# Performance work log

Measured on AMD Instinct MI355X. Metric: run time of the kernel, lower is better.

## Reference

```python
import jax, jax.numpy as jnp
import numpy as np

B, J, E = 4096, 32, 256

def setup_inputs() -> dict:
    key = jax.random.key(0)
    ks = jax.random.split(key, 7)
    return {
        "x": jax.random.normal(ks[0], (B, E), dtype=jnp.float32),
        "state": jax.random.normal(ks[1], (B, J * E), dtype=jnp.float32),
        "keys": jax.random.normal(ks[2], (J, E), dtype=jnp.float32) * 0.1,
        "U": jax.random.normal(ks[3], (E, E), dtype=jnp.float32) * 0.1,
        "V": jax.random.normal(ks[4], (E, E), dtype=jnp.float32) * 0.1,
        "W": jax.random.normal(ks[5], (E, E), dtype=jnp.float32) * 0.1,
        "bias": jax.random.normal(ks[6], (E,), dtype=jnp.float32) * 0.1,
    }

def reference(x, state, keys, U, V, W, bias):
    b, je = state.shape
    j = keys.shape[0]
    e = x.shape[1]
    s = state.reshape(b, j, e)                      # [B,J,E]
    # gate_j = sigmoid(<x, state_j> + <x, key_j>)
    gate = jax.nn.sigmoid(jnp.einsum('be,bje->bj', x, s)
                          + x @ keys.T)             # [B,J]
    # candidate_j = relu(U s_j + bias + W x + V k_j)
    cand = jax.nn.relu(jnp.einsum('bje,fe->bjf', s, U)
                       + bias
                       + (x @ W.T)[:, None, :]
                       + (keys @ V.T)[None, :, :])  # [B,J,E]
    s_next = s + gate[..., None] * cand
    norm = jnp.abs(jnp.linalg.norm(s_next, axis=-1, keepdims=True)) + 1e-8
    s_next = s_next / norm
    return s_next.reshape(b, je)
```

## Files before the change

kernel.cpp:

```cpp
#include <hip/hip_runtime.h>
#include <hip/hip_bf16.h>

typedef __bf16 bf16_t;
typedef __attribute__((ext_vector_type(8))) __bf16 bf16x8;
typedef __attribute__((ext_vector_type(4))) float f32x4;

#define E_DIM 256
#define J_DIM 32
#define B_DIM 4096
#define M_DIM (B_DIM * J_DIM)
#define BM 64
#define BK 32
#define LDA 40
#define LDB 40
#define LDAF 33

#define XK_LDA (E_DIM + 4)

__device__ inline bf16x8 cvt8(const float* __restrict__ p) {
    f32x4 a = *(const f32x4*)p;
    f32x4 b = *(const f32x4*)(p + 4);
    bf16x8 r;
    r[0] = (bf16_t)a[0]; r[1] = (bf16_t)a[1]; r[2] = (bf16_t)a[2]; r[3] = (bf16_t)a[3];
    r[4] = (bf16_t)b[0]; r[5] = (bf16_t)b[1]; r[6] = (bf16_t)b[2]; r[7] = (bf16_t)b[3];
    return r;
}

__global__ __launch_bounds__(256) void xkvkb_kernel(
    const float* __restrict__ x, const float* __restrict__ keys,
    const float* __restrict__ V, const float* __restrict__ bias,
    float* __restrict__ xk, float* __restrict__ vkb) {
    __shared__ float smem[(J_DIM + 8) * XK_LDA];
    int tid = threadIdx.x, bid = blockIdx.x;
    if (bid < 512) {
        float* sK = smem;
        float* sX = smem + J_DIM * XK_LDA;
        int b0 = bid * 8;
#pragma unroll
        for (int it = 0; it < 8; ++it) {
            int t = it * 256 + tid;
            int r = t >> 6, c = (t & 63) * 4;
            *(f32x4*)(sK + r * XK_LDA + c) = *(const f32x4*)(keys + (size_t)r * E_DIM + c);
        }
#pragma unroll
        for (int it = 0; it < 2; ++it) {
            int t = it * 256 + tid;
            int r = t >> 6, c = (t & 63) * 4;
            *(f32x4*)(sX + r * XK_LDA + c) =
                *(const f32x4*)(x + (size_t)b0 * E_DIM + (size_t)r * E_DIM + c);
        }
        __syncthreads();
        int j = tid & 31, bl = tid >> 5;
        float acc = 0.f;
        for (int e = 0; e < E_DIM; e += 4) {
            f32x4 xv = *(const f32x4*)(sX + bl * XK_LDA + e);
            f32x4 kv = *(const f32x4*)(sK + j * XK_LDA + e);
#pragma unroll
            for (int i = 0; i < 4; ++i) acc += xv[i] * kv[i];
        }
        xk[(size_t)(b0 + bl) * J_DIM + j] = acc;
    } else {
        int j = bid - 512, f = tid;
        float* sk = smem;
        sk[f] = keys[(size_t)j * E_DIM + f];
        __syncthreads();
        float acc = bias[f];
        for (int e = 0; e < E_DIM; e += 4) {
            f32x4 vv = *(const f32x4*)(V + (size_t)f * E_DIM + e);
#pragma unroll
            for (int i = 0; i < 4; ++i) acc += vv[i] * sk[e + i];
        }
        vkb[(size_t)j * E_DIM + f] = acc;
    }
}

__global__ __launch_bounds__(256) void wx_kernel(const float* __restrict__ x,
                                                 const float* __restrict__ W,
                                                 float* __restrict__ wx) {
    __shared__ __align__(16) bf16_t sA[BM][LDA];
    __shared__ __align__(16) bf16_t sBw[64][LDB];
    int tid = threadIdx.x;
    int w = tid >> 6, lane = tid & 63, quad = lane >> 4, l15 = lane & 15;
    int m0 = (blockIdx.x >> 2) * BM, n0 = (blockIdx.x & 3) * 64;
    f32x4 acc[4];
#pragma unroll
    for (int nt = 0; nt < 4; ++nt)
#pragma unroll
        for (int r = 0; r < 4; ++r) acc[nt][r] = 0.f;
    int arow = tid >> 2, akk = (tid & 3) * 8;
    for (int kc = 0; kc < 8; ++kc) {
        int k0 = kc * BK;
        __syncthreads();
        *(bf16x8*)(&sA[arow][akk]) = cvt8(x + (size_t)(m0 + arow) * E_DIM + k0 + akk);
        *(bf16x8*)(&sBw[arow][akk]) = cvt8(W + (size_t)(n0 + arow) * E_DIM + k0 + akk);
        __syncthreads();
        bf16x8 af = *(const bf16x8*)(&sA[w * 16 + l15][quad * 8]);
#pragma unroll
        for (int nt = 0; nt < 4; ++nt) {
            bf16x8 bfr = *(const bf16x8*)(&sBw[nt * 16 + l15][quad * 8]);
            acc[nt] = __builtin_amdgcn_mfma_f32_16x16x32_bf16(af, bfr, acc[nt], 0, 0, 0);
        }
    }
#pragma unroll
    for (int nt = 0; nt < 4; ++nt)
#pragma unroll
        for (int r = 0; r < 4; ++r)
            wx[(size_t)(m0 + w * 16 + quad * 4 + r) * E_DIM + n0 + nt * 16 + l15] =
                acc[nt][r];
}

__global__ __launch_bounds__(256) void memcell_kernel(
    const float* __restrict__ x, const float* __restrict__ state,
    const float* __restrict__ U, const float* __restrict__ wx,
    const float* __restrict__ xk, const float* __restrict__ vkb,
    float* __restrict__ out) {
    __shared__ __align__(16) bf16_t sA[BM][LDA];
    __shared__ __align__(16) bf16_t sB[E_DIM][LDB];
    __shared__ __align__(16) float sAf[BM][LDAF];
    __shared__ __align__(16) float sXf[2][E_DIM];
    int tid = threadIdx.x;
    int w = tid >> 6, lane = tid & 63, quad = lane >> 4, l15 = lane & 15;
    int m0 = blockIdx.x * BM;
    int b0 = m0 >> 5;
    f32x4 acc[16];
#pragma unroll
    for (int nt = 0; nt < 16; ++nt)
#pragma unroll
        for (int r = 0; r < 4; ++r) acc[nt][r] = 0.f;
    float gdot = 0.f;
    if (tid < 64) {
        int bb = tid >> 5, p = tid & 31;
        f32x4 xa = *(const f32x4*)(x + (size_t)(b0 + bb) * E_DIM + p * 8);
        f32x4 xb = *(const f32x4*)(x + (size_t)(b0 + bb) * E_DIM + p * 8 + 4);
        *(f32x4*)(&sXf[bb][p * 8]) = xa;
        *(f32x4*)(&sXf[bb][p * 8 + 4]) = xb;
    }
    int arow = tid >> 2, akk = (tid & 3) * 8;
    for (int kc = 0; kc < 8; ++kc) {
        int k0 = kc * BK;
        __syncthreads();
        {
            const float* sp = state + (size_t)(m0 + arow) * E_DIM + k0 + akk;
            f32x4 a = *(const f32x4*)sp;
            f32x4 b = *(const f32x4*)(sp + 4);
            *(f32x4*)(&sAf[arow][akk]) = a;
            *(f32x4*)(&sAf[arow][akk + 4]) = b;
            bf16x8 r;
            r[0] = (bf16_t)a[0]; r[1] = (bf16_t)a[1]; r[2] = (bf16_t)a[2]; r[3] = (bf16_t)a[3];
            r[4] = (bf16_t)b[0]; r[5] = (bf16_t)b[1]; r[6] = (bf16_t)b[2]; r[7] = (bf16_t)b[3];
            *(bf16x8*)(&sA[arow][akk]) = r;
        }
#pragma unroll
        for (int it = 0; it < 4; ++it) {
            int t = it * 256 + tid;
            int n = t >> 2, kk = (t & 3) * 8;
            *(bf16x8*)(&sB[n][kk]) = cvt8(U + (size_t)n * E_DIM + k0 + kk);
        }
        __syncthreads();
        bf16x8 af = *(const bf16x8*)(&sA[w * 16 + l15][quad * 8]);
#pragma unroll
        for (int i = 0; i < 8; ++i)
            gdot += sAf[w * 16 + l15][quad * 8 + i] * sXf[w >> 1][k0 + quad * 8 + i];
#pragma unroll
        for (int nt = 0; nt < 16; ++nt) {
            bf16x8 bfr = *(const bf16x8*)(&sB[nt * 16 + l15][quad * 8]);
            acc[nt] = __builtin_amdgcn_mfma_f32_16x16x32_bf16(af, bfr, acc[nt], 0, 0, 0);
        }
    }
    gdot += __shfl_xor(gdot, 16);
    gdot += __shfl_xor(gdot, 32);
    int bw = b0 + (w >> 1);
    float garg = gdot + xk[(size_t)bw * J_DIM + (w & 1) * 16 + l15];
    float gv = 1.f / (1.f + expf(-garg));
    float gate[4];
#pragma unroll
    for (int r = 0; r < 4; ++r) gate[r] = __shfl(gv, quad * 4 + r);
    float sumsq[4] = {0.f, 0.f, 0.f, 0.f};
    const float* wxrow = wx + (size_t)bw * E_DIM;
#pragma unroll
    for (int nt = 0; nt < 16; ++nt) {
        int f = nt * 16 + l15;
        float wxf = wxrow[f];
#pragma unroll
        for (int r = 0; r < 4; ++r) {
            int rl = quad * 4 + r;
            int jidx = (w & 1) * 16 + rl;
            float c = acc[nt][r] + wxf + vkb[(size_t)jidx * E_DIM + f];
            c = fmaxf(c, 0.f);
            float sv = state[(size_t)(m0 + w * 16 + rl) * E_DIM + f];
            float t = fmaf(gate[r], c, sv);
            acc[nt][r] = t;
            sumsq[r] += t * t;
        }
    }
    float rn[4];
#pragma unroll
    for (int r = 0; r < 4; ++r) {
        float s2 = sumsq[r];
        s2 += __shfl_xor(s2, 1);
        s2 += __shfl_xor(s2, 2);
        s2 += __shfl_xor(s2, 4);
        s2 += __shfl_xor(s2, 8);
        rn[r] = 1.f / (sqrtf(s2) + 1e-8f);
    }
#pragma unroll
    for (int nt = 0; nt < 16; ++nt)
#pragma unroll
        for (int r = 0; r < 4; ++r)
            out[(size_t)(m0 + w * 16 + quad * 4 + r) * E_DIM + nt * 16 + l15] =
                acc[nt][r] * rn[r];
}

extern "C" void kernel_launch(void* const* d_in, const int* in_sizes, int n_in,
                              void* d_out, int out_size, void* d_ws, size_t ws_size,
                              hipStream_t stream) {
    const float* x     = (const float*)d_in[0];
    const float* state = (const float*)d_in[1];
    const float* keys  = (const float*)d_in[2];
    const float* U     = (const float*)d_in[3];
    const float* V     = (const float*)d_in[4];
    const float* W     = (const float*)d_in[5];
    const float* bias  = (const float*)d_in[6];
    float* out = (float*)d_out;

    float* wsf = (float*)d_ws;
    float* wx  = wsf;
    float* xk  = wsf + (size_t)B_DIM * E_DIM;
    float* vkb = xk + (size_t)B_DIM * J_DIM;

    xkvkb_kernel<<<544, 256, 0, stream>>>(x, keys, V, bias, xk, vkb);
    wx_kernel<<<256, 256, 0, stream>>>(x, W, wx);
    memcell_kernel<<<M_DIM / BM, 256, 0, stream>>>(x, state, U, wx, xk, vkb, out);
}
```

Baseline: 309.4 us.

## Pre-convert U to bf16 once and register-prefetch next K tile in memcell

U is now converted to bf16 once per call by extra blocks in the small precompute kernel, so each memcell block loads ready bf16 data instead of converting fp32 U on every K step. The memcell main loop also software-pipelines its loads: the next K chunk of state and U is fetched into registers while the MFMAs for the current chunk run, then written to shared memory between barriers. This is meant to hide global memory latency and drop redundant conversions, at the cost of higher register pressure that may reduce occupancy.

Result: no change. 314.6 us (+1.7%).

```diff
diff --git a/kernel.cpp b/kernel.cpp
--- a/kernel.cpp
+++ b/kernel.cpp
@@ -3,6 +3,7 @@
 
 typedef __bf16 bf16_t;
 typedef __attribute__((ext_vector_type(8))) __bf16 bf16x8;
+typedef __attribute__((ext_vector_type(4))) __bf16 bf16x4;
 typedef __attribute__((ext_vector_type(4))) float f32x4;
 
 #define E_DIM 256
@@ -28,8 +29,9 @@
 
 __global__ __launch_bounds__(256) void xkvkb_kernel(
     const float* __restrict__ x, const float* __restrict__ keys,
-    const float* __restrict__ V, const float* __restrict__ bias,
-    float* __restrict__ xk, float* __restrict__ vkb) {
+    const float* __restrict__ U, const float* __restrict__ V,
+    const float* __restrict__ bias,
+    float* __restrict__ xk, float* __restrict__ vkb, bf16_t* __restrict__ Ubf) {
     __shared__ float smem[(J_DIM + 8) * XK_LDA];
     int tid = threadIdx.x, bid = blockIdx.x;
     if (bid < 512) {
@@ -59,8 +61,15 @@
             for (int i = 0; i < 4; ++i) acc += xv[i] * kv[i];
         }
         xk[(size_t)(b0 + bl) * J_DIM + j] = acc;
+    } else if (bid < 576) {
+        int idx = (bid - 512) * 1024 + tid * 4;
+        f32x4 v = *(const f32x4*)(U + idx);
+        bf16x4 o;
+#pragma unroll
+        for (int i = 0; i < 4; ++i) o[i] = (bf16_t)v[i];
+        *(bf16x4*)(Ubf + idx) = o;
     } else {
-        int j = bid - 512, f = tid;
+        int j = bid - 576, f = tid;
         float* sk = smem;
         sk[f] = keys[(size_t)j * E_DIM + f];
         __syncthreads();
@@ -111,7 +120,7 @@
 
 __global__ __launch_bounds__(256) void memcell_kernel(
     const float* __restrict__ x, const float* __restrict__ state,
-    const float* __restrict__ U, const float* __restrict__ wx,
+    const bf16_t* __restrict__ Ubf, const float* __restrict__ wx,
     const float* __restrict__ xk, const float* __restrict__ vkb,
     float* __restrict__ out) {
     __shared__ __align__(16) bf16_t sA[BM][LDA];
@@ -136,27 +145,44 @@
         *(f32x4*)(&sXf[bb][p * 8 + 4]) = xb;
     }
     int arow = tid >> 2, akk = (tid & 3) * 8;
+    const float* astage = state + (size_t)(m0 + arow) * E_DIM + akk;
+
+    f32x4 pa0 = *(const f32x4*)(astage);
+    f32x4 pa1 = *(const f32x4*)(astage + 4);
+    bf16x8 pb0, pb1, pb2, pb3;
+    {
+        const bf16_t* up = Ubf + (size_t)(tid >> 2) * E_DIM + akk;
+        pb0 = *(const bf16x8*)(up);
+        pb1 = *(const bf16x8*)(up + 64 * E_DIM);
+        pb2 = *(const bf16x8*)(up + 128 * E_DIM);
+        pb3 = *(const bf16x8*)(up + 192 * E_DIM);
+    }
+    {
+        *(f32x4*)(&sAf[arow][akk]) = pa0;
+        *(f32x4*)(&sAf[arow][akk + 4]) = pa1;
+        bf16x8 r;
+        r[0] = (bf16_t)pa0[0]; r[1] = (bf16_t)pa0[1]; r[2] = (bf16_t)pa0[2]; r[3] = (bf16_t)pa0[3];
+        r[4] = (bf16_t)pa1[0]; r[5] = (bf16_t)pa1[1]; r[6] = (bf16_t)pa1[2]; r[7] = (bf16_t)pa1[3];
+        *(bf16x8*)(&sA[arow][akk]) = r;
+        *(bf16x8*)(&sB[arow][akk]) = pb0;
+        *(bf16x8*)(&sB[64 + arow][akk]) = pb1;
+        *(bf16x8*)(&sB[128 + arow][akk]) = pb2;
+        *(bf16x8*)(&sB[192 + arow][akk]) = pb3;
+    }
+    __syncthreads();
+
     for (int kc = 0; kc < 8; ++kc) {
+        if (kc < 7) {
+            int k0n = (kc + 1) * BK;
+            pa0 = *(const f32x4*)(astage + k0n);
+            pa1 = *(const f32x4*)(astage + k0n + 4);
+            const bf16_t* up = Ubf + (size_t)(tid >> 2) * E_DIM + k0n + akk;
+            pb0 = *(const bf16x8*)(up);
+            pb1 = *(const bf16x8*)(up + 64 * E_DIM);
+            pb2 = *(const bf16x8*)(up + 128 * E_DIM);
+            pb3 = *(const bf16x8*)(up + 192 * E_DIM);
+        }
         int k0 = kc * BK;
-        __syncthreads();
-        {
-            const float* sp = state + (size_t)(m0 + arow) * E_DIM + k0 + akk;
-            f32x4 a = *(const f32x4*)sp;
-            f32x4 b = *(const f32x4*)(sp + 4);
-            *(f32x4*)(&sAf[arow][akk]) = a;
-            *(f32x4*)(&sAf[arow][akk + 4]) = b;
-            bf16x8 r;
-            r[0] = (bf16_t)a[0]; r[1] = (bf16_t)a[1]; r[2] = (bf16_t)a[2]; r[3] = (bf16_t)a[3];
-            r[4] = (bf16_t)b[0]; r[5] = (bf16_t)b[1]; r[6] = (bf16_t)b[2]; r[7] = (bf16_t)b[3];
-            *(bf16x8*)(&sA[arow][akk]) = r;
-        }
-#pragma unroll
-        for (int it = 0; it < 4; ++it) {
-            int t = it * 256 + tid;
-            int n = t >> 2, kk = (t & 3) * 8;
-            *(bf16x8*)(&sB[n][kk]) = cvt8(U + (size_t)n * E_DIM + k0 + kk);
-        }
-        __syncthreads();
         bf16x8 af = *(const bf16x8*)(&sA[w * 16 + l15][quad * 8]);
 #pragma unroll
         for (int i = 0; i < 8; ++i)
@@ -166,6 +192,20 @@
             bf16x8 bfr = *(const bf16x8*)(&sB[nt * 16 + l15][quad * 8]);
             acc[nt] = __builtin_amdgcn_mfma_f32_16x16x32_bf16(af, bfr, acc[nt], 0, 0, 0);
         }
+        __syncthreads();
+        if (kc < 7) {
+            *(f32x4*)(&sAf[arow][akk]) = pa0;
+            *(f32x4*)(&sAf[arow][akk + 4]) = pa1;
+            bf16x8 r;
+            r[0] = (bf16_t)pa0[0]; r[1] = (bf16_t)pa0[1]; r[2] = (bf16_t)pa0[2]; r[3] = (bf16_t)pa0[3];
+            r[4] = (bf16_t)pa1[0]; r[5] = (bf16_t)pa1[1]; r[6] = (bf16_t)pa1[2]; r[7] = (bf16_t)pa1[3];
+            *(bf16x8*)(&sA[arow][akk]) = r;
+            *(bf16x8*)(&sB[arow][akk]) = pb0;
+            *(bf16x8*)(&sB[64 + arow][akk]) = pb1;
+            *(bf16x8*)(&sB[128 + arow][akk]) = pb2;
+            *(bf16x8*)(&sB[192 + arow][akk]) = pb3;
+        }
+        __syncthreads();
     }
     gdot += __shfl_xor(gdot, 16);
     gdot += __shfl_xor(gdot, 32);
@@ -227,8 +267,9 @@
     float* wx  = wsf;
     float* xk  = wsf + (size_t)B_DIM * E_DIM;
     float* vkb = xk + (size_t)B_DIM * J_DIM;
-
-    xkvkb_kernel<<<544, 256, 0, stream>>>(x, keys, V, bias, xk, vkb);
+    bf16_t* Ubf = (bf16_t*)(vkb + (size_t)J_DIM * E_DIM);
+
+    xkvkb_kernel<<<608, 256, 0, stream>>>(x, keys, U, V, bias, xk, vkb, Ubf);
     wx_kernel<<<256, 256, 0, stream>>>(x, W, wx);
-    memcell_kernel<<<M_DIM / BM, 256, 0, stream>>>(x, state, U, wx, xk, vkb, out);
-}
+    memcell_kernel<<<M_DIM / BM, 256, 0, stream>>>(x, state, Ubf, wx, xk, vkb, out);
+}
```

## Pre-convert U to bf16 once and stream it into LDS via global_load_lds with XOR swizzle

Applied to the files above, without the earlier changes.

U is now converted to bf16 once in the prologue kernel and kept in workspace, so each memcell block no longer reloads fp32 U and converts it per K-chunk. Tiles of U are copied straight into LDS with the async global_load_lds builtin, and the padding is replaced by an XOR swizzle to avoid bank conflicts. This halves the bytes read for U and removes VALU conversion work from the main loop. The cost is one extra small conversion pass, plus reliance on the direct-to-LDS load layout being correct.

New measurement: 355.6 us. 14.9% more time.

```diff
diff --git a/kernel.cpp b/kernel.cpp
--- a/kernel.cpp
+++ b/kernel.cpp
@@ -3,6 +3,7 @@
 
 typedef __bf16 bf16_t;
 typedef __attribute__((ext_vector_type(8))) __bf16 bf16x8;
+typedef __attribute__((ext_vector_type(4))) __bf16 bf16x4;
 typedef __attribute__((ext_vector_type(4))) float f32x4;
 
 #define E_DIM 256
@@ -28,8 +29,9 @@
 
 __global__ __launch_bounds__(256) void xkvkb_kernel(
     const float* __restrict__ x, const float* __restrict__ keys,
-    const float* __restrict__ V, const float* __restrict__ bias,
-    float* __restrict__ xk, float* __restrict__ vkb) {
+    const float* __restrict__ U, const float* __restrict__ V,
+    const float* __restrict__ bias,
+    float* __restrict__ xk, float* __restrict__ vkb, bf16_t* __restrict__ Ubf) {
     __shared__ float smem[(J_DIM + 8) * XK_LDA];
     int tid = threadIdx.x, bid = blockIdx.x;
     if (bid < 512) {
@@ -59,8 +61,15 @@
             for (int i = 0; i < 4; ++i) acc += xv[i] * kv[i];
         }
         xk[(size_t)(b0 + bl) * J_DIM + j] = acc;
+    } else if (bid < 576) {
+        int idx = (bid - 512) * 1024 + tid * 4;
+        f32x4 v = *(const f32x4*)(U + idx);
+        bf16x4 o;
+#pragma unroll
+        for (int i = 0; i < 4; ++i) o[i] = (bf16_t)v[i];
+        *(bf16x4*)(Ubf + idx) = o;
     } else {
-        int j = bid - 512, f = tid;
+        int j = bid - 576, f = tid;
         float* sk = smem;
         sk[f] = keys[(size_t)j * E_DIM + f];
         __syncthreads();
@@ -77,11 +86,11 @@
 __global__ __launch_bounds__(256) void wx_kernel(const float* __restrict__ x,
                                                  const float* __restrict__ W,
                                                  float* __restrict__ wx) {
-    __shared__ __align__(16) bf16_t sA[BM][LDA];
+    __shared__ __align__(16) bf16_t sA[64][LDA];
     __shared__ __align__(16) bf16_t sBw[64][LDB];
     int tid = threadIdx.x;
     int w = tid >> 6, lane = tid & 63, quad = lane >> 4, l15 = lane & 15;
-    int m0 = (blockIdx.x >> 2) * BM, n0 = (blockIdx.x & 3) * 64;
+    int m0 = (blockIdx.x >> 2) * 64, n0 = (blockIdx.x & 3) * 64;
     f32x4 acc[4];
 #pragma unroll
     for (int nt = 0; nt < 4; ++nt)
@@ -111,11 +120,11 @@
 
 __global__ __launch_bounds__(256) void memcell_kernel(
     const float* __restrict__ x, const float* __restrict__ state,
-    const float* __restrict__ U, const float* __restrict__ wx,
+    const bf16_t* __restrict__ Ubf, const float* __restrict__ wx,
     const float* __restrict__ xk, const float* __restrict__ vkb,
     float* __restrict__ out) {
     __shared__ __align__(16) bf16_t sA[BM][LDA];
-    __shared__ __align__(16) bf16_t sB[E_DIM][LDB];
+    __shared__ __align__(16) bf16_t sB[E_DIM][32];
     __shared__ __align__(16) float sAf[BM][LDAF];
     __shared__ __align__(16) float sXf[2][E_DIM];
     int tid = threadIdx.x;
@@ -136,6 +145,8 @@
         *(f32x4*)(&sXf[bb][p * 8 + 4]) = xb;
     }
     int arow = tid >> 2, akk = (tid & 3) * 8;
+    bf16_t* lbase = &sB[0][0];
+    int bswz = (l15 >> 1) & 3;
     for (int kc = 0; kc < 8; ++kc) {
         int k0 = kc * BK;
         __syncthreads();
@@ -152,18 +163,24 @@
         }
 #pragma unroll
         for (int it = 0; it < 4; ++it) {
-            int t = it * 256 + tid;
-            int n = t >> 2, kk = (t & 3) * 8;
-            *(bf16x8*)(&sB[n][kk]) = cvt8(U + (size_t)n * E_DIM + k0 + kk);
+            int s = it * 256 + tid;
+            int n = s >> 2, kk = s & 3;
+            int kksrc = kk ^ ((n >> 1) & 3);
+            const bf16_t* g = Ubf + (size_t)n * E_DIM + k0 + kksrc * 8;
+            __builtin_amdgcn_global_load_lds(
+                (const __attribute__((address_space(1))) unsigned int*)g,
+                (__attribute__((address_space(3))) unsigned int*)(lbase + s * 8),
+                16, 0, 0);
         }
         __syncthreads();
         bf16x8 af = *(const bf16x8*)(&sA[w * 16 + l15][quad * 8]);
 #pragma unroll
         for (int i = 0; i < 8; ++i)
             gdot += sAf[w * 16 + l15][quad * 8 + i] * sXf[w >> 1][k0 + quad * 8 + i];
+        int qs = (quad ^ bswz) * 8;
 #pragma unroll
         for (int nt = 0; nt < 16; ++nt) {
-            bf16x8 bfr = *(const bf16x8*)(&sB[nt * 16 + l15][quad * 8]);
+            bf16x8 bfr = *(const bf16x8*)(&sB[nt * 16 + l15][qs]);
             acc[nt] = __builtin_amdgcn_mfma_f32_16x16x32_bf16(af, bfr, acc[nt], 0, 0, 0);
         }
     }
@@ -227,8 +244,9 @@
     float* wx  = wsf;
     float* xk  = wsf + (size_t)B_DIM * E_DIM;
     float* vkb = xk + (size_t)B_DIM * J_DIM;
-
-    xkvkb_kernel<<<544, 256, 0, stream>>>(x, keys, V, bias, xk, vkb);
+    bf16_t* Ubf = (bf16_t*)(vkb + (size_t)J_DIM * E_DIM);
+
+    xkvkb_kernel<<<608, 256, 0, stream>>>(x, keys, U, V, bias, xk, vkb, Ubf);
     wx_kernel<<<256, 256, 0, stream>>>(x, W, wx);
-    memcell_kernel<<<M_DIM / BM, 256, 0, stream>>>(x, state, U, wx, xk, vkb, out);
-}
+    memcell_kernel<<<M_DIM / BM, 256, 0, stream>>>(x, state, Ubf, wx, xk, vkb, out);
+}
```

## Merge prep kernels into one launch and compute gate dot from registers

Applied to the files above, without the earlier changes.

Folds the Wx GEMM blocks into the xk/vkb prep kernel so the preprocessing runs as one launch instead of two. In the main kernel, the fp32 shared-memory copy of the state tile is removed. Each thread now accumulates the gate dot product from the state values it already loaded, then reduces across the four threads that share a row. This cuts shared-memory traffic and footprint, which may raise occupancy, at the cost of different shuffle patterns and branch divergence in the merged kernel.

After: 299.6 us. 1.03x faster.

```diff
diff --git a/kernel.cpp b/kernel.cpp
--- a/kernel.cpp
+++ b/kernel.cpp
@@ -13,7 +13,6 @@
 #define BK 32
 #define LDA 40
 #define LDB 40
-#define LDAF 33
 
 #define XK_LDA (E_DIM + 4)
 
@@ -26,11 +25,12 @@
     return r;
 }
 
-__global__ __launch_bounds__(256) void xkvkb_kernel(
+__global__ __launch_bounds__(256) void prep_kernel(
     const float* __restrict__ x, const float* __restrict__ keys,
     const float* __restrict__ V, const float* __restrict__ bias,
-    float* __restrict__ xk, float* __restrict__ vkb) {
-    __shared__ float smem[(J_DIM + 8) * XK_LDA];
+    const float* __restrict__ W,
+    float* __restrict__ xk, float* __restrict__ vkb, float* __restrict__ wx) {
+    __shared__ __align__(16) float smem[(J_DIM + 8) * XK_LDA];
     int tid = threadIdx.x, bid = blockIdx.x;
     if (bid < 512) {
         float* sK = smem;
@@ -59,7 +59,7 @@
             for (int i = 0; i < 4; ++i) acc += xv[i] * kv[i];
         }
         xk[(size_t)(b0 + bl) * J_DIM + j] = acc;
-    } else {
+    } else if (bid < 544) {
         int j = bid - 512, f = tid;
         float* sk = smem;
         sk[f] = keys[(size_t)j * E_DIM + f];
@@ -71,42 +71,38 @@
             for (int i = 0; i < 4; ++i) acc += vv[i] * sk[e + i];
         }
         vkb[(size_t)j * E_DIM + f] = acc;
-    }
-}
-
-__global__ __launch_bounds__(256) void wx_kernel(const float* __restrict__ x,
-                                                 const float* __restrict__ W,
-                                                 float* __restrict__ wx) {
-    __shared__ __align__(16) bf16_t sA[BM][LDA];
-    __shared__ __align__(16) bf16_t sBw[64][LDB];
-    int tid = threadIdx.x;
-    int w = tid >> 6, lane = tid & 63, quad = lane >> 4, l15 = lane & 15;
-    int m0 = (blockIdx.x >> 2) * BM, n0 = (blockIdx.x & 3) * 64;
-    f32x4 acc[4];
-#pragma unroll
-    for (int nt = 0; nt < 4; ++nt)
-#pragma unroll
-        for (int r = 0; r < 4; ++r) acc[nt][r] = 0.f;
-    int arow = tid >> 2, akk = (tid & 3) * 8;
-    for (int kc = 0; kc < 8; ++kc) {
-        int k0 = kc * BK;
-        __syncthreads();
-        *(bf16x8*)(&sA[arow][akk]) = cvt8(x + (size_t)(m0 + arow) * E_DIM + k0 + akk);
-        *(bf16x8*)(&sBw[arow][akk]) = cvt8(W + (size_t)(n0 + arow) * E_DIM + k0 + akk);
-        __syncthreads();
-        bf16x8 af = *(const bf16x8*)(&sA[w * 16 + l15][quad * 8]);
-#pragma unroll
-        for (int nt = 0; nt < 4; ++nt) {
-            bf16x8 bfr = *(const bf16x8*)(&sBw[nt * 16 + l15][quad * 8]);
-            acc[nt] = __builtin_amdgcn_mfma_f32_16x16x32_bf16(af, bfr, acc[nt], 0, 0, 0);
-        }
-    }
-#pragma unroll
-    for (int nt = 0; nt < 4; ++nt)
-#pragma unroll
-        for (int r = 0; r < 4; ++r)
-            wx[(size_t)(m0 + w * 16 + quad * 4 + r) * E_DIM + n0 + nt * 16 + l15] =
-                acc[nt][r];
+    } else {
+        bf16_t (*sA)[LDA]  = (bf16_t (*)[LDA])smem;
+        bf16_t (*sBw)[LDB] = (bf16_t (*)[LDB])(smem + 1280);
+        int w = tid >> 6, lane = tid & 63, quad = lane >> 4, l15 = lane & 15;
+        int wbid = bid - 544;
+        int m0 = (wbid >> 2) * 64, n0 = (wbid & 3) * 64;
+        f32x4 acc[4];
+#pragma unroll
+        for (int nt = 0; nt < 4; ++nt)
+#pragma unroll
+            for (int r = 0; r < 4; ++r) acc[nt][r] = 0.f;
+        int arow = tid >> 2, akk = (tid & 3) * 8;
+        for (int kc = 0; kc < 8; ++kc) {
+            int k0 = kc * BK;
+            __syncthreads();
+            *(bf16x8*)(&sA[arow][akk]) = cvt8(x + (size_t)(m0 + arow) * E_DIM + k0 + akk);
+            *(bf16x8*)(&sBw[arow][akk]) = cvt8(W + (size_t)(n0 + arow) * E_DIM + k0 + akk);
+            __syncthreads();
+            bf16x8 af = *(const bf16x8*)(&sA[w * 16 + l15][quad * 8]);
+#pragma unroll
+            for (int nt = 0; nt < 4; ++nt) {
+                bf16x8 bfr = *(const bf16x8*)(&sBw[nt * 16 + l15][quad * 8]);
+                acc[nt] = __builtin_amdgcn_mfma_f32_16x16x32_bf16(af, bfr, acc[nt], 0, 0, 0);
+            }
+        }
+#pragma unroll
+        for (int nt = 0; nt < 4; ++nt)
+#pragma unroll
+            for (int r = 0; r < 4; ++r)
+                wx[(size_t)(m0 + w * 16 + quad * 4 + r) * E_DIM + n0 + nt * 16 + l15] =
+                    acc[nt][r];
+    }
 }
 
 __global__ __launch_bounds__(256) void memcell_kernel(
@@ -116,7 +112,6 @@
     float* __restrict__ out) {
     __shared__ __align__(16) bf16_t sA[BM][LDA];
     __shared__ __align__(16) bf16_t sB[E_DIM][LDB];
-    __shared__ __align__(16) float sAf[BM][LDAF];
     __shared__ __align__(16) float sXf[2][E_DIM];
     int tid = threadIdx.x;
     int w = tid >> 6, lane = tid & 63, quad = lane >> 4, l15 = lane & 15;
@@ -127,7 +122,7 @@
     for (int nt = 0; nt < 16; ++nt)
 #pragma unroll
         for (int r = 0; r < 4; ++r) acc[nt][r] = 0.f;
-    float gdot = 0.f;
+    float gpart = 0.f;
     if (tid < 64) {
         int bb = tid >> 5, p = tid & 31;
         f32x4 xa = *(const f32x4*)(x + (size_t)(b0 + bb) * E_DIM + p * 8);
@@ -136,6 +131,7 @@
         *(f32x4*)(&sXf[bb][p * 8 + 4]) = xb;
     }
     int arow = tid >> 2, akk = (tid & 3) * 8;
+    const float* xrow = &sXf[arow >> 5][0];
     for (int kc = 0; kc < 8; ++kc) {
         int k0 = kc * BK;
         __syncthreads();
@@ -143,12 +139,14 @@
             const float* sp = state + (size_t)(m0 + arow) * E_DIM + k0 + akk;
             f32x4 a = *(const f32x4*)sp;
             f32x4 b = *(const f32x4*)(sp + 4);
-            *(f32x4*)(&sAf[arow][akk]) = a;
-            *(f32x4*)(&sAf[arow][akk + 4]) = b;
             bf16x8 r;
             r[0] = (bf16_t)a[0]; r[1] = (bf16_t)a[1]; r[2] = (bf16_t)a[2]; r[3] = (bf16_t)a[3];
             r[4] = (bf16_t)b[0]; r[5] = (bf16_t)b[1]; r[6] = (bf16_t)b[2]; r[7] = (bf16_t)b[3];
             *(bf16x8*)(&sA[arow][akk]) = r;
+#pragma unroll
+            for (int i = 0; i < 4; ++i) gpart += a[i] * xrow[k0 + akk + i];
+#pragma unroll
+            for (int i = 0; i < 4; ++i) gpart += b[i] * xrow[k0 + akk + 4 + i];
         }
 #pragma unroll
         for (int it = 0; it < 4; ++it) {
@@ -159,22 +157,20 @@
         __syncthreads();
         bf16x8 af = *(const bf16x8*)(&sA[w * 16 + l15][quad * 8]);
 #pragma unroll
-        for (int i = 0; i < 8; ++i)
-            gdot += sAf[w * 16 + l15][quad * 8 + i] * sXf[w >> 1][k0 + quad * 8 + i];
-#pragma unroll
         for (int nt = 0; nt < 16; ++nt) {
             bf16x8 bfr = *(const bf16x8*)(&sB[nt * 16 + l15][quad * 8]);
             acc[nt] = __builtin_amdgcn_mfma_f32_16x16x32_bf16(af, bfr, acc[nt], 0, 0, 0);
         }
     }
-    gdot += __shfl_xor(gdot, 16);
-    gdot += __shfl_xor(gdot, 32);
+    gpart += __shfl_xor(gpart, 1);
+    gpart += __shfl_xor(gpart, 2);
     int bw = b0 + (w >> 1);
-    float garg = gdot + xk[(size_t)bw * J_DIM + (w & 1) * 16 + l15];
+    int jrow = (w & 1) * 16 + (arow & 15);
+    float garg = gpart + xk[(size_t)bw * J_DIM + jrow];
     float gv = 1.f / (1.f + expf(-garg));
     float gate[4];
 #pragma unroll
-    for (int r = 0; r < 4; ++r) gate[r] = __shfl(gv, quad * 4 + r);
+    for (int r = 0; r < 4; ++r) gate[r] = __shfl(gv, (quad * 4 + r) * 4);
     float sumsq[4] = {0.f, 0.f, 0.f, 0.f};
     const float* wxrow = wx + (size_t)bw * E_DIM;
 #pragma unroll
@@ -228,7 +224,6 @@
     float* xk  = wsf + (size_t)B_DIM * E_DIM;
     float* vkb = xk + (size_t)B_DIM * J_DIM;
 
-    xkvkb_kernel<<<544, 256, 0, stream>>>(x, keys, V, bias, xk, vkb);
-    wx_kernel<<<256, 256, 0, stream>>>(x, W, wx);
+    prep_kernel<<<800, 256, 0, stream>>>(x, keys, V, bias, W, xk, vkb, wx);
     memcell_kernel<<<M_DIM / BM, 256, 0, stream>>>(x, state, U, wx, xk, vkb, out);
 }
```
